# Performance work log

Hardware: AMD Instinct MI355X
Metric: run time of the kernel (lower is better)

Reference implementation:

```python
import jax, jax.numpy as jnp
import numpy as np

NEG_SLOPE = 0.2  # PyG GATConv default
LN_EPS = 1e-5

B, N, DIN, H, DH, DOUT = 256, 256, 128, 4, 32, 1


def setup_inputs() -> dict:
    key = jax.random.key(0)
    ks = jax.random.split(key, 12)
    s = lambda *shape: 0.1
    return {
        "x": jax.random.normal(ks[0], (B, N, DIN), jnp.float32),
        "adj": jnp.ones((B, N, N), jnp.float32),  # unused (graph is fully connected)
        # GATConv 1: dim_in -> H heads x DH
        "W1": jax.random.normal(ks[1], (DIN, H * DH), jnp.float32) * 0.05,
        "b1": jnp.zeros((H * DH,), jnp.float32),
        "att_src1": jax.random.normal(ks[2], (H, DH), jnp.float32) * 0.1,
        "att_dst1": jax.random.normal(ks[3], (H, DH), jnp.float32) * 0.1,
        # LayerNorm over hidden dim H*DH
        "gamma": jnp.ones((H * DH,), jnp.float32),
        "beta": jnp.zeros((H * DH,), jnp.float32),
        # GATConv 2: H*DH -> 1 head x DOUT, concat=False
        "W2": jax.random.normal(ks[4], (H * DH, DOUT), jnp.float32) * 0.05,
        "b2": jnp.zeros((DOUT,), jnp.float32),
        "att_src2": jax.random.normal(ks[5], (1, DOUT), jnp.float32) * 0.1,
        "att_dst2": jax.random.normal(ks[6], (1, DOUT), jnp.float32) * 0.1,
    }


def _gat_layer(x, W, b, att_src, att_dst):
    """Dense GATConv on a fully-connected graph.
    x: [B, N, Fin] -> out: [B, N, H, D], attn: [B, H, N, N].
    Node i aggregates over all j: e_ij = leaky_relu(a_dst.h_i + a_src.h_j).
    """
    Hh, D = att_src.shape
    h = (x @ W).reshape(x.shape[0], x.shape[1], Hh, D)          # [B,N,H,D]
    a_src = jnp.einsum("bnhd,hd->bnh", h, att_src)              # neighbor term
    a_dst = jnp.einsum("bnhd,hd->bnh", h, att_dst)              # central term
    e = a_dst.transpose(0, 2, 1)[:, :, :, None] + a_src.transpose(0, 2, 1)[:, :, None, :]  # [B,H,N,N]
    e = jax.nn.leaky_relu(e, NEG_SLOPE)
    attn = jax.nn.softmax(e, axis=-1)                           # softmax over neighbors j
    out = jnp.einsum("bhij,bjhd->bihd", attn, h)                # [B,N,H,D]
    return out, attn, b


def reference(x, adj, W1, b1, att_src1, att_dst1, gamma, beta, W2, b2, att_src2, att_dst2):
    del adj  # module ignores adj; graph is fully connected
    # layer 1: concat heads
    h1, _, _ = _gat_layer(x, W1, b1, att_src1, att_dst1)
    h1 = h1.reshape(B, N, H * DH) + b1                          # [B,N,H*DH]
    # LayerNorm over hidden dim
    mu = jnp.mean(h1, axis=-1, keepdims=True)
    var = jnp.mean(jnp.square(h1 - mu), axis=-1, keepdims=True)
    h1 = (h1 - mu) * jax.lax.rsqrt(var + LN_EPS) * gamma + beta
    # layer 2: single head, concat=False (mean over 1 head == identity)
    h2, attn2, _ = _gat_layer(h1, W2, b2, att_src2, att_dst2)
    h2 = h2.reshape(B, N, DOUT) + b2
    out = jax.nn.elu(h2)                                        # [B,N,DOUT]
    return out
```

## Files before the change

### kernel.cpp

```cpp
#include <hip/hip_runtime.h>
#include <hip/hip_bf16.h>
#include <math.h>

#define BB 256
#define NN 256
#define DIN 128
#define NH 4
#define DH 32
#define HID 128
#define NEG 0.2f
#define LN_EPS 1e-5f
#define L2E 1.44269504f

typedef __hip_bfloat16 bf16;
typedef __attribute__((ext_vector_type(8))) short short8;
typedef __attribute__((ext_vector_type(4))) float float4v;
typedef __attribute__((ext_vector_type(2))) unsigned int uint2v;
typedef __attribute__((ext_vector_type(4))) unsigned int uint4v;

__device__ __forceinline__ float s2f(short s) {
    return __uint_as_float(((unsigned int)(unsigned short)s) << 16);
}
__device__ __forceinline__ short f2bs(float f) {
    return (short)((__float_as_uint(f) + 0x8000u) >> 16);
}
__device__ __forceinline__ unsigned int pack2(float a, float b) {
    return __builtin_amdgcn_perm(__float_as_uint(b) + 0x8000u,
                                 __float_as_uint(a) + 0x8000u, 0x07060302u);
}
__device__ __forceinline__ float lrelu(float x) { return fmaxf(x, NEG * x); }

#define MFMA16(a, b, c) __builtin_amdgcn_mfma_f32_16x16x32_bf16(a, b, c, 0, 0, 0)

__global__ __launch_bounds__(1024) void k_mega(
    const float* __restrict__ x, const float* __restrict__ W1,
    const float* __restrict__ as1, const float* __restrict__ ad1,
    const float* __restrict__ b1, const float* __restrict__ gamma,
    const float* __restrict__ beta, const float* __restrict__ W2,
    const float* __restrict__ bias2, const float* __restrict__ att_src2,
    const float* __restrict__ att_dst2, float* __restrict__ out)
{
    const int b = blockIdx.x, t = threadIdx.x;
    const int w = t >> 6, lane = t & 63;
    const int l16 = lane & 15, q = lane >> 4;

    __shared__ short uA[34816];
    __shared__ short hR[34816];
    __shared__ float Bs[NH][NN], Bsp[NH][NN], dd[NH][NN];
    __shared__ float b1s[HID], gws[HID], bws[HID], atts[HID], attd[HID];
    __shared__ float Ssc[2];
    __shared__ float h2v[NN], svv[NN];

    const float* xb = x + (size_t)b * NN * DIN;
#pragma unroll
    for (int it = 0; it < 8; ++it) {
        const int idx = t + it * 1024;
        const int row = idx >> 5, c4 = idx & 31;
        const float4v v = ((const float4v*)xb)[idx];
        uint2v p;
        p[0] = pack2(v[0], v[1]);
        p[1] = pack2(v[2], v[3]);
        *(uint2v*)&uA[row * 136 + c4 * 4] = p;
    }
    {
        const int n = t & 127, kc = t >> 7, k0 = kc * 16;
        float v[16];
#pragma unroll
        for (int e = 0; e < 16; ++e) v[e] = W1[(k0 + e) * HID + n];
        uint4v pa, pb;
#pragma unroll
        for (int e = 0; e < 4; ++e) {
            pa[e] = pack2(v[2 * e], v[2 * e + 1]);
            pb[e] = pack2(v[8 + 2 * e], v[9 + 2 * e]);
        }
        *(uint4v*)&hR[n * 136 + k0] = pa;
        *(uint4v*)&hR[n * 136 + k0 + 8] = pb;
    }
    if (t < HID) {
        b1s[t] = b1[t];
        const float w2v = W2[t];
        gws[t] = gamma[t] * w2v;
        bws[t] = beta[t] * w2v;
        atts[t] = as1[t] * L2E;
        attd[t] = ad1[t] * L2E;
    }
    __syncthreads();

    const int dtile = w & 7, jhalf = w >> 3;
    float4v acc1[8];
#pragma unroll
    for (int i = 0; i < 8; ++i) acc1[i] = (float4v){0.f, 0.f, 0.f, 0.f};
    const short* arow = &hR[(dtile * 16 + l16) * 136];
#pragma unroll
    for (int ks = 0; ks < 4; ++ks) {
        const short8 afr = *(const short8*)&arow[ks * 32 + q * 8];
#pragma unroll
        for (int nt = 0; nt < 8; ++nt) {
            const short8 bfr = *(const short8*)&uA[((jhalf * 8 + nt) * 16 + l16) * 136 + ks * 32 + q * 8];
            acc1[nt] = MFMA16(afr, bfr, acc1[nt]);
        }
    }
    __syncthreads();
#pragma unroll
    for (int nt = 0; nt < 8; ++nt)
#pragma unroll
        for (int r = 0; r < 4; ++r)
            uA[(dtile * 16 + q * 4 + r) * 264 + (jhalf * 8 + nt) * 16 + l16] = f2bs(acc1[nt][r]);
    __syncthreads();

    {
        const int hs = t >> 8, js = t & 255;
        float vs = 0.f, vd = 0.f;
#pragma unroll 8
        for (int d2 = 0; d2 < 32; ++d2) {
            const float hv = s2f(uA[(hs * 32 + d2) * 264 + js]);
            vs = fmaf(hv, atts[hs * 32 + d2], vs);
            vd = fmaf(hv, attd[hs * 32 + d2], vd);
        }
        Bs[hs][js]  = exp2f(vs);
        Bsp[hs][js] = exp2f(NEG * vs);
        dd[hs][js]  = vd;
    }
    __syncthreads();

    {
        if (w < 2) {
            const float* src = (w == 0) ? gws : bws;
            float v = src[lane] + src[lane + 64];
#pragma unroll
            for (int m = 1; m < 64; m <<= 1) v += __shfl_xor(v, m, 64);
            if (lane == 0) Ssc[w] = v;
        }
        const int hh = w >> 2, qtr = w & 3;
        float Au[4], Apu[4], Tu[4];
#pragma unroll
        for (int u = 0; u < 4; ++u) {
            const float dv = dd[hh][qtr * 64 + u * 16 + l16];
            Au[u]  = exp2f(dv);
            Apu[u] = exp2f(NEG * dv);
            Tu[u]  = exp2f(-dv);
        }
        float4v acc2[4][2], accL[4];
#pragma unroll
        for (int u = 0; u < 4; ++u) {
            acc2[u][0] = (float4v){0.f, 0.f, 0.f, 0.f};
            acc2[u][1] = (float4v){0.f, 0.f, 0.f, 0.f};
            accL[u]    = (float4v){0.f, 0.f, 0.f, 0.f};
        }
        short8 ones;
#pragma unroll
        for (int e = 0; e < 8; ++e) ones[e] = (short)0x3F80;

        const short* hTh = &uA[(hh * 32) * 264];
#pragma unroll 2
        for (int ks = 0; ks < 8; ++ks) {
            const short8 a0 = *(const short8*)&hTh[l16 * 264 + ks * 32 + q * 8];
            const short8 a1 = *(const short8*)&hTh[(16 + l16) * 264 + ks * 32 + q * 8];
            const float4v bs0 = *(const float4v*)&Bs[hh][ks * 32 + q * 8];
            const float4v bs1 = *(const float4v*)&Bs[hh][ks * 32 + q * 8 + 4];
            const float4v bp0 = *(const float4v*)&Bsp[hh][ks * 32 + q * 8];
            const float4v bp1 = *(const float4v*)&Bsp[hh][ks * 32 + q * 8 + 4];
            const float bsj[8] = {bs0[0], bs0[1], bs0[2], bs0[3], bs1[0], bs1[1], bs1[2], bs1[3]};
            const float bpj[8] = {bp0[0], bp0[1], bp0[2], bp0[3], bp1[0], bp1[1], bp1[2], bp1[3]};
#pragma unroll
            for (int u = 0; u < 4; ++u) {
                union { short8 s8; unsigned int u32[4]; } bfr;
#pragma unroll
                for (int p = 0; p < 4; ++p) {
                    const bool c0 = bsj[2 * p]     >= Tu[u];
                    const bool c1 = bsj[2 * p + 1] >= Tu[u];
                    const float w0 = (c0 ? Au[u] : Apu[u]) * (c0 ? bsj[2 * p]     : bpj[2 * p]);
                    const float w1 = (c1 ? Au[u] : Apu[u]) * (c1 ? bsj[2 * p + 1] : bpj[2 * p + 1]);
                    bfr.u32[p] = pack2(w0, w1);
                }
                acc2[u][0] = MFMA16(a0, bfr.s8, acc2[u][0]);
                acc2[u][1] = MFMA16(a1, bfr.s8, acc2[u][1]);
                accL[u]    = MFMA16(ones, bfr.s8, accL[u]);
            }
        }
#pragma unroll
        for (int u = 0; u < 4; ++u) {
            const float inv = 1.f / accL[u][0];
            const int i = qtr * 64 + u * 16 + l16;
#pragma unroll
            for (int mt = 0; mt < 2; ++mt)
#pragma unroll
                for (int r = 0; r < 4; ++r)
                    hR[(hh * 32 + mt * 16 + q * 4 + r) * 264 + i] = f2bs(acc2[u][mt][r] * inv);
        }
    }
    __syncthreads();

    float* pw = (float*)uA;
    const int i3 = t & 255, hf = t >> 8;
    {
        float s = 0.f, sq = 0.f, t3 = 0.f;
#pragma unroll 8
        for (int dz = 0; dz < 32; ++dz) {
            const int d = hf * 32 + dz;
            const float v = s2f(hR[d * 264 + i3]) + b1s[d];
            s += v;
            sq = fmaf(v, v, sq);
            t3 = fmaf(v, gws[d], t3);
        }
        const int pbase = (hf * 256 + i3) * 3;
        pw[pbase] = s; pw[pbase + 1] = sq; pw[pbase + 2] = t3;
        __syncthreads();
        if (hf == 0) {
            for (int k = 1; k < 4; ++k) {
                const int pb = (k * 256 + i3) * 3;
                s += pw[pb]; sq += pw[pb + 1]; t3 += pw[pb + 2];
            }
            const float mu = s * (1.f / HID);
            const float var = sq * (1.f / HID) - mu * mu;
            const float rs = rsqrtf(var + LN_EPS);
            const float h2 = rs * (t3 - mu * Ssc[0]) + Ssc[1];
            h2v[i3] = h2;
            svv[i3] = h2 * att_src2[0];
        }
    }
    __syncthreads();

    {
        const float di = h2v[i3] * att_dst2[0];
        float mloc = -1e30f;
#pragma unroll 4
        for (int jz = 0; jz < 64; ++jz)
            mloc = fmaxf(mloc, lrelu(di + svv[hf * 64 + jz]));
        pw[4096 + hf * 256 + i3] = mloc;
        __syncthreads();
        float mfin = pw[4096 + i3];
#pragma unroll
        for (int k = 1; k < 4; ++k) mfin = fmaxf(mfin, pw[4096 + k * 256 + i3]);
        float l2 = 0.f, num = 0.f;
#pragma unroll 4
        for (int jz = 0; jz < 64; ++jz) {
            const int j = hf * 64 + jz;
            const float wgt = __expf(lrelu(di + svv[j]) - mfin);
            l2 += wgt;
            num = fmaf(wgt, h2v[j], num);
        }
        const int qb = 5120 + (hf * 256 + i3) * 2;
        pw[qb] = l2; pw[qb + 1] = num;
        __syncthreads();
        if (hf == 0) {
#pragma unroll
            for (int k = 1; k < 4; ++k) {
                const int pb = 5120 + (k * 256 + i3) * 2;
                l2 += pw[pb]; num += pw[pb + 1];
            }
            float o = num / l2 + bias2[0];
            o = (o > 0.f) ? o : (__expf(o) - 1.f);
            out[b * NN + i3] = o;
        }
    }
}

extern "C" void kernel_launch(void* const* d_in, const int* in_sizes, int n_in,
                              void* d_out, int out_size, void* d_ws, size_t ws_size,
                              hipStream_t stream) {
    const float* x   = (const float*)d_in[0];
    const float* W1  = (const float*)d_in[2];
    const float* b1  = (const float*)d_in[3];
    const float* as1 = (const float*)d_in[4];
    const float* ad1 = (const float*)d_in[5];
    const float* gam = (const float*)d_in[6];
    const float* bet = (const float*)d_in[7];
    const float* W2  = (const float*)d_in[8];
    const float* bi2 = (const float*)d_in[9];
    const float* as2 = (const float*)d_in[10];
    const float* ad2 = (const float*)d_in[11];
    float* out = (float*)d_out;

    k_mega<<<BB, 1024, 0, stream>>>(x, W1, as1, ad1, b1, gam, bet, W2,
                                    bi2, as2, ad2, out);
}
```

Baseline: 152.9 us.

## Fold attention vectors into W1 GEMM, fuse LayerNorm stats, drop max pass

Precomputes W1·att_src/att_dst as extra MFMA rows so two waves produce the attention logits alongside the projection GEMM, replacing a separate LDS pass. The leaky-relu select is rewritten as a max of two exponential products. LayerNorm partial sums are computed from the GEMM accumulators via shuffles instead of writing hR back to LDS. The layer-2 softmax drops its max-subtraction pass and uses factored exponentials, which risks overflow for large logits. The launch bound gains a min-blocks hint, which can add register pressure.

```diff
diff --git a/kernel.cpp b/kernel.cpp
--- a/kernel.cpp
+++ b/kernel.cpp
@@ -12,15 +12,11 @@
 #define LN_EPS 1e-5f
 #define L2E 1.44269504f
 
-typedef __hip_bfloat16 bf16;
 typedef __attribute__((ext_vector_type(8))) short short8;
 typedef __attribute__((ext_vector_type(4))) float float4v;
 typedef __attribute__((ext_vector_type(2))) unsigned int uint2v;
 typedef __attribute__((ext_vector_type(4))) unsigned int uint4v;
 
-__device__ __forceinline__ float s2f(short s) {
-    return __uint_as_float(((unsigned int)(unsigned short)s) << 16);
-}
 __device__ __forceinline__ short f2bs(float f) {
     return (short)((__float_as_uint(f) + 0x8000u) >> 16);
 }
@@ -28,11 +24,10 @@
     return __builtin_amdgcn_perm(__float_as_uint(b) + 0x8000u,
                                  __float_as_uint(a) + 0x8000u, 0x07060302u);
 }
-__device__ __forceinline__ float lrelu(float x) { return fmaxf(x, NEG * x); }
 
 #define MFMA16(a, b, c) __builtin_amdgcn_mfma_f32_16x16x32_bf16(a, b, c, 0, 0, 0)
 
-__global__ __launch_bounds__(1024) void k_mega(
+__global__ __launch_bounds__(1024, 4) void k_mega(
     const float* __restrict__ x, const float* __restrict__ W1,
     const float* __restrict__ as1, const float* __restrict__ ad1,
     const float* __restrict__ b1, const float* __restrict__ gamma,
@@ -45,11 +40,14 @@
     const int l16 = lane & 15, q = lane >> 4;
 
     __shared__ short uA[34816];
-    __shared__ short hR[34816];
-    __shared__ float Bs[NH][NN], Bsp[NH][NN], dd[NH][NN];
-    __shared__ float b1s[HID], gws[HID], bws[HID], atts[HID], attd[HID];
+    __shared__ short W1Ts[128 * 136];
+    __shared__ short awT[16 * 136];
+    __shared__ float Bs[NH][NN], Bsp[NH][NN];
+    __shared__ float ssraw[NH][NN], ddlog[NH][NN];
+    __shared__ float b1s[HID], gws[HID], bws[HID];
+    __shared__ float part[NH][NN * 3];
     __shared__ float Ssc[2];
-    __shared__ float h2v[NN], svv[NN];
+    __shared__ float h2v[NN], Ej[NN], Epj[NN];
 
     const float* xb = x + (size_t)b * NN * DIN;
 #pragma unroll
@@ -73,32 +71,60 @@
             pa[e] = pack2(v[2 * e], v[2 * e + 1]);
             pb[e] = pack2(v[8 + 2 * e], v[9 + 2 * e]);
         }
-        *(uint4v*)&hR[n * 136 + k0] = pa;
-        *(uint4v*)&hR[n * 136 + k0 + 8] = pb;
+        *(uint4v*)&W1Ts[n * 136 + k0] = pa;
+        *(uint4v*)&W1Ts[n * 136 + k0 + 8] = pb;
+    }
+    {
+        const int rr = t >> 7, k = t & 127;
+        const int hh = rr & 3;
+        const float* att = ((rr & 4) ? ad1 : as1) + hh * 32;
+        const float* wrow = W1 + k * HID + hh * 32;
+        float acc = 0.f;
+#pragma unroll
+        for (int e = 0; e < 8; ++e) {
+            const float4v wv = *(const float4v*)(wrow + e * 4);
+            const float4v av = *(const float4v*)(att + e * 4);
+            acc += wv[0] * av[0] + wv[1] * av[1] + wv[2] * av[2] + wv[3] * av[3];
+        }
+        awT[rr * 136 + k] = f2bs(acc * L2E);
     }
     if (t < HID) {
         b1s[t] = b1[t];
         const float w2v = W2[t];
         gws[t] = gamma[t] * w2v;
         bws[t] = beta[t] * w2v;
-        atts[t] = as1[t] * L2E;
-        attd[t] = ad1[t] * L2E;
     }
     __syncthreads();
 
     const int dtile = w & 7, jhalf = w >> 3;
-    float4v acc1[8];
-#pragma unroll
-    for (int i = 0; i < 8; ++i) acc1[i] = (float4v){0.f, 0.f, 0.f, 0.f};
-    const short* arow = &hR[(dtile * 16 + l16) * 136];
+    const bool isaug = (w == 0) || (w == 15);
+    float4v acc1[8], accA[8];
+#pragma unroll
+    for (int i = 0; i < 8; ++i) {
+        acc1[i] = (float4v){0.f, 0.f, 0.f, 0.f};
+        accA[i] = (float4v){0.f, 0.f, 0.f, 0.f};
+    }
+    const short* arow = &W1Ts[(dtile * 16 + l16) * 136];
+    const short* arow2 = &awT[l16 * 136];
 #pragma unroll
     for (int ks = 0; ks < 4; ++ks) {
         const short8 afr = *(const short8*)&arow[ks * 32 + q * 8];
+        short8 afr2;
+        if (isaug) afr2 = *(const short8*)&arow2[ks * 32 + q * 8];
 #pragma unroll
         for (int nt = 0; nt < 8; ++nt) {
             const short8 bfr = *(const short8*)&uA[((jhalf * 8 + nt) * 16 + l16) * 136 + ks * 32 + q * 8];
             acc1[nt] = MFMA16(afr, bfr, acc1[nt]);
-        }
+            if (isaug) accA[nt] = MFMA16(afr2, bfr, accA[nt]);
+        }
+    }
+    if (isaug && q < 2) {
+        float (*dstA)[NN] = (q == 0) ? ssraw : ddlog;
+#pragma unroll
+        for (int nt = 0; nt < 8; ++nt)
+#pragma unroll
+            for (int r = 0; r < 4; ++r)
+                dstA[r][jhalf * 128 + nt * 16 + l16] = accA[nt][r];
     }
     __syncthreads();
 #pragma unroll
@@ -106,20 +132,11 @@
 #pragma unroll
         for (int r = 0; r < 4; ++r)
             uA[(dtile * 16 + q * 4 + r) * 264 + (jhalf * 8 + nt) * 16 + l16] = f2bs(acc1[nt][r]);
-    __syncthreads();
-
     {
         const int hs = t >> 8, js = t & 255;
-        float vs = 0.f, vd = 0.f;
-#pragma unroll 8
-        for (int d2 = 0; d2 < 32; ++d2) {
-            const float hv = s2f(uA[(hs * 32 + d2) * 264 + js]);
-            vs = fmaf(hv, atts[hs * 32 + d2], vs);
-            vd = fmaf(hv, attd[hs * 32 + d2], vd);
-        }
-        Bs[hs][js]  = exp2f(vs);
+        const float vs = ssraw[hs][js];
+        Bs[hs][js] = exp2f(vs);
         Bsp[hs][js] = exp2f(NEG * vs);
-        dd[hs][js]  = vd;
     }
     __syncthreads();
 
@@ -132,13 +149,12 @@
             if (lane == 0) Ssc[w] = v;
         }
         const int hh = w >> 2, qtr = w & 3;
-        float Au[4], Apu[4], Tu[4];
+        float Au[4], Apu[4];
 #pragma unroll
         for (int u = 0; u < 4; ++u) {
-            const float dv = dd[hh][qtr * 64 + u * 16 + l16];
-            Au[u]  = exp2f(dv);
+            const float dv = ddlog[hh][qtr * 64 + u * 16 + l16];
+            Au[u] = exp2f(dv);
             Apu[u] = exp2f(NEG * dv);
-            Tu[u]  = exp2f(-dv);
         }
         float4v acc2[4][2], accL[4];
 #pragma unroll
@@ -167,10 +183,8 @@
                 union { short8 s8; unsigned int u32[4]; } bfr;
 #pragma unroll
                 for (int p = 0; p < 4; ++p) {
-                    const bool c0 = bsj[2 * p]     >= Tu[u];
-                    const bool c1 = bsj[2 * p + 1] >= Tu[u];
-                    const float w0 = (c0 ? Au[u] : Apu[u]) * (c0 ? bsj[2 * p]     : bpj[2 * p]);
-                    const float w1 = (c1 ? Au[u] : Apu[u]) * (c1 ? bsj[2 * p + 1] : bpj[2 * p + 1]);
+                    const float w0 = fmaxf(Au[u] * bsj[2 * p],     Apu[u] * bpj[2 * p]);
+                    const float w1 = fmaxf(Au[u] * bsj[2 * p + 1], Apu[u] * bpj[2 * p + 1]);
                     bfr.u32[p] = pack2(w0, w1);
                 }
                 acc2[u][0] = MFMA16(a0, bfr.s8, acc2[u][0]);
@@ -178,76 +192,78 @@
                 accL[u]    = MFMA16(ones, bfr.s8, accL[u]);
             }
         }
+        float b1r[8], gwr[8];
+#pragma unroll
+        for (int mt = 0; mt < 2; ++mt)
+#pragma unroll
+            for (int r = 0; r < 4; ++r) {
+                const int d = hh * 32 + mt * 16 + q * 4 + r;
+                b1r[mt * 4 + r] = b1s[d];
+                gwr[mt * 4 + r] = gws[d];
+            }
 #pragma unroll
         for (int u = 0; u < 4; ++u) {
             const float inv = 1.f / accL[u][0];
-            const int i = qtr * 64 + u * 16 + l16;
+            float s = 0.f, sq = 0.f, t3 = 0.f;
 #pragma unroll
             for (int mt = 0; mt < 2; ++mt)
 #pragma unroll
-                for (int r = 0; r < 4; ++r)
-                    hR[(hh * 32 + mt * 16 + q * 4 + r) * 264 + i] = f2bs(acc2[u][mt][r] * inv);
-        }
-    }
-    __syncthreads();
-
-    float* pw = (float*)uA;
-    const int i3 = t & 255, hf = t >> 8;
-    {
+                for (int r = 0; r < 4; ++r) {
+                    const float v = fmaf(acc2[u][mt][r], inv, b1r[mt * 4 + r]);
+                    s += v;
+                    sq = fmaf(v, v, sq);
+                    t3 = fmaf(v, gwr[mt * 4 + r], t3);
+                }
+            s  += __shfl_xor(s, 16, 64);  s  += __shfl_xor(s, 32, 64);
+            sq += __shfl_xor(sq, 16, 64); sq += __shfl_xor(sq, 32, 64);
+            t3 += __shfl_xor(t3, 16, 64); t3 += __shfl_xor(t3, 32, 64);
+            if (q == 0) {
+                float* pp = &part[hh][(qtr * 64 + u * 16 + l16) * 3];
+                pp[0] = s; pp[1] = sq; pp[2] = t3;
+            }
+        }
+    }
+    __syncthreads();
+
+    if (t < NN) {
         float s = 0.f, sq = 0.f, t3 = 0.f;
-#pragma unroll 8
-        for (int dz = 0; dz < 32; ++dz) {
-            const int d = hf * 32 + dz;
-            const float v = s2f(hR[d * 264 + i3]) + b1s[d];
-            s += v;
-            sq = fmaf(v, v, sq);
-            t3 = fmaf(v, gws[d], t3);
-        }
-        const int pbase = (hf * 256 + i3) * 3;
-        pw[pbase] = s; pw[pbase + 1] = sq; pw[pbase + 2] = t3;
-        __syncthreads();
-        if (hf == 0) {
-            for (int k = 1; k < 4; ++k) {
-                const int pb = (k * 256 + i3) * 3;
-                s += pw[pb]; sq += pw[pb + 1]; t3 += pw[pb + 2];
-            }
-            const float mu = s * (1.f / HID);
-            const float var = sq * (1.f / HID) - mu * mu;
-            const float rs = rsqrtf(var + LN_EPS);
-            const float h2 = rs * (t3 - mu * Ssc[0]) + Ssc[1];
-            h2v[i3] = h2;
-            svv[i3] = h2 * att_src2[0];
-        }
-    }
-    __syncthreads();
-
-    {
-        const float di = h2v[i3] * att_dst2[0];
-        float mloc = -1e30f;
-#pragma unroll 4
-        for (int jz = 0; jz < 64; ++jz)
-            mloc = fmaxf(mloc, lrelu(di + svv[hf * 64 + jz]));
-        pw[4096 + hf * 256 + i3] = mloc;
-        __syncthreads();
-        float mfin = pw[4096 + i3];
-#pragma unroll
-        for (int k = 1; k < 4; ++k) mfin = fmaxf(mfin, pw[4096 + k * 256 + i3]);
+#pragma unroll
+        for (int hh2 = 0; hh2 < 4; ++hh2) {
+            const float* pp = &part[hh2][t * 3];
+            s += pp[0]; sq += pp[1]; t3 += pp[2];
+        }
+        const float mu = s * (1.f / HID);
+        const float var = sq * (1.f / HID) - mu * mu;
+        const float rs = rsqrtf(var + LN_EPS);
+        const float h2 = rs * (t3 - mu * Ssc[0]) + Ssc[1];
+        h2v[t] = h2;
+        const float e = h2 * att_src2[0];
+        Ej[t]  = __expf(e);
+        Epj[t] = __expf(NEG * e);
+    }
+    __syncthreads();
+
+    {
+        const int i3 = t & 255, hf = t >> 8;
+        const float ed = h2v[i3] * att_dst2[0];
+        const float Di = __expf(ed), Dip = __expf(NEG * ed);
         float l2 = 0.f, num = 0.f;
 #pragma unroll 4
         for (int jz = 0; jz < 64; ++jz) {
             const int j = hf * 64 + jz;
-            const float wgt = __expf(lrelu(di + svv[j]) - mfin);
+            const float wgt = fmaxf(Di * Ej[j], Dip * Epj[j]);
             l2 += wgt;
             num = fmaf(wgt, h2v[j], num);
         }
-        const int qb = 5120 + (hf * 256 + i3) * 2;
-        pw[qb] = l2; pw[qb + 1] = num;
+        float* pw = &part[0][0];
+        const int pb = (hf * 256 + i3) * 2;
+        pw[pb] = l2; pw[pb + 1] = num;
         __syncthreads();
         if (hf == 0) {
 #pragma unroll
             for (int k = 1; k < 4; ++k) {
-                const int pb = 5120 + (k * 256 + i3) * 2;
-                l2 += pw[pb]; num += pw[pb + 1];
+                const int pk = (k * 256 + i3) * 2;
+                l2 += pw[pk]; num += pw[pk + 1];
             }
             float o = num / l2 + bias2[0];
             o = (o > 0.f) ? o : (__expf(o) - 1.f);
```

New measurement: 146.4 us. -4.3%, faster.
